# Kernel tuning notes

Hardware: AMD Instinct MI355X
Metric: run time of the kernel (lower is better)

## Reference

```python
import jax, jax.numpy as jnp
import numpy as np

EPS_NORM = 1e-12  # F.normalize eps
EPS_BN = 1e-5     # BatchNorm2d eps


def _neighbor_idx(h, w):
    # Replicates get_window_mask's clamped 3x3 neighbor indices (hw, 9).
    off = np.array([-1, 0, 1])
    x_off = np.tile(off, 3)        # [-1,0,1,-1,0,1,-1,0,1]
    y_off = np.repeat(off, 3)      # [-1,-1,-1,0,0,0,1,1,1]
    yy, xx = np.meshgrid(np.arange(h), np.arange(w), indexing='ij')
    x_nn = np.clip(xx.reshape(-1, 1) + x_off[None, :], 0, w - 1)
    y_nn = np.clip(yy.reshape(-1, 1) + y_off[None, :], 0, h - 1)
    return jnp.asarray(y_nn * w + x_nn, dtype=jnp.int32)  # (hw, 9)


def _find_nn(xf, yf, idx):
    # Faithful to find_nn: cosine sim between cur pixel and 3x3 window of y,
    # argmin over the (masked-in) window, gather the NORMALIZED y feature.
    # The dense (hw,hw) matmul + 9999 mask reduces exactly to these 9 candidates.
    b, c, h, w = xf.shape
    xn = xf.reshape(b, c, h * w).transpose(0, 2, 1)  # (b, hw, c)
    xn = xn / jnp.maximum(jnp.linalg.norm(xn, axis=-1, keepdims=True), EPS_NORM)
    yn = yf.reshape(b, c, h * w)
    yn = yn / jnp.maximum(jnp.linalg.norm(yn, axis=1, keepdims=True), EPS_NORM)
    ynt = yn.transpose(0, 2, 1)          # (b, hw, c)
    y_nb = ynt[:, idx, :]                # (b, hw, 9, c) gathered neighbors
    sims = jnp.einsum('bpc,bpkc->bpk', xn, y_nb)  # (b, hw, 9)
    k = jnp.argmin(sims, axis=-1)
    nnv = jnp.take_along_axis(y_nb, k[:, :, None, None], axis=2)[:, :, 0, :]
    return nnv.transpose(0, 2, 1).reshape(b, c, h, w)


def _forward(x, conv_w, bn_gamma, bn_beta):
    h, w = x.shape[-2:]
    prev_f, next_f, cur_f = x[:, 0], x[:, 1], x[:, 2]
    idx = _neighbor_idx(h, w)
    nn_prev = _find_nn(cur_f, prev_f, idx)
    nn_next = _find_nn(cur_f, next_f, idx)
    feat = jnp.concatenate([nn_prev, nn_next, cur_f], axis=1)  # (b, 3c, h, w)
    out = jnp.einsum('oc,bchw->bohw', conv_w, feat)            # 1x1 conv, no bias
    # BatchNorm2d in training mode: per-channel batch stats (biased var)
    mean = out.mean(axis=(0, 2, 3), keepdims=True)
    var = out.var(axis=(0, 2, 3), keepdims=True)
    out = (out - mean) * jax.lax.rsqrt(var + EPS_BN)
    out = out * bn_gamma[None, :, None, None] + bn_beta[None, :, None, None]
    out = jax.nn.relu(out)
    return jnp.stack([prev_f, next_f, out], axis=1)  # (b, 3, c, h, w)


def setup_inputs() -> dict:
    key = jax.random.key(0)
    k1, k2 = jax.random.split(key)
    b, c, h, w = 8, 256, 64, 64
    x = jax.random.normal(k1, (b, 3, c, h, w), dtype=jnp.float32)
    fan_in, fan_out = 3 * c, c
    bound = float(np.sqrt(6.0 / (fan_in + fan_out)))  # xavier_uniform
    conv_w = jax.random.uniform(k2, (c, 3 * c), dtype=jnp.float32, minval=-bound, maxval=bound)
    bn_gamma = jnp.ones((c,), dtype=jnp.float32)
    bn_beta = jnp.zeros((c,), dtype=jnp.float32)
    return {'x': x, 'conv_w': conv_w, 'bn_gamma': bn_gamma, 'bn_beta': bn_beta}


def reference(x, conv_w, bn_gamma, bn_beta):
    return _forward(x, conv_w, bn_gamma, bn_beta)
```

## Files before the change

kernel.cpp:

```cpp
#include <hip/hip_runtime.h>

constexpr int B  = 8;
constexpr int C  = 256;
constexpr int Hh = 64;
constexpr int Ww = 64;
constexpr int P  = Hh * Ww;
constexpr int CP = C * P;
constexpr int CT = 3 * C;
constexpr int J  = B * P;

constexpr int DOT_D_OFF = 0;
constexpr int SSQ_D_OFF = 294912;
constexpr int IV_F_OFF  = 655360;
constexpr int SEL_F_OFF = 663552;
constexpr int SIV_F_OFF = 671744;
constexpr int WB_F_OFF  = 679936;

typedef __attribute__((ext_vector_type(8))) short short8;
typedef __attribute__((ext_vector_type(4))) float f32x4;

__device__ inline unsigned short bf16_rne(float f) {
    unsigned u = __float_as_uint(f);
    return (unsigned short)((u + 0x7fffu + ((u >> 16) & 1u)) >> 16);
}
__device__ inline unsigned pack2(float a, float b) {
    return (unsigned)bf16_rne(a) | ((unsigned)bf16_rne(b) << 16);
}

__global__ __launch_bounds__(256) void k_wcvt(const float* __restrict__ Wg,
                                              unsigned short* __restrict__ Wb) {
    int i = blockIdx.x * 256 + threadIdx.x;
    Wb[i] = bf16_rne(Wg[i]);
}

__global__ __launch_bounds__(256) void k_dots(const float* __restrict__ x,
                                              float* __restrict__ out) {
    __shared__ float ys[2][2][6][64];
    __shared__ float cs[2][256];
    const int t     = threadIdx.x;
    const int b     = blockIdx.x >> 4;
    const int strip = blockIdx.x & 15;
    const int chunk = blockIdx.y;
    const int y0 = strip * 4;
    const int ry = t >> 6;
    const int xc = t & 63;
    const int xm = max(xc - 1, 0), xp = min(xc + 1, 63);
    const int c0 = chunk * 64;

    size_t gbase; int l0;
    if (t < 64) {
        gbase = (size_t)(b * 3 + 2) * CP + (size_t)c0 * P + strip * 256 + t * 4;
        l0 = t * 4;
    } else {
        int i   = t - 64;
        int sid = i >= 96;
        int r   = (i - sid * 96) >> 4;
        int x4  = i & 15;
        int yl  = min(max(y0 - 1 + r, 0), Hh - 1);
        gbase = (size_t)(b * 3 + sid) * CP + (size_t)c0 * P + yl * 64 + x4 * 4;
        l0 = (sid * 6 + r) * 64 + x4 * 4;
    }
    float* ysf = &ys[0][0][0][0];
    float* dst0 = (t < 64) ? &cs[0][l0] : &ysf[l0];
    float* dst1 = (t < 64) ? &cs[1][l0] : &ysf[768 + l0];

    double d[2][9] = {{0,0,0,0,0,0,0,0,0},{0,0,0,0,0,0,0,0,0}};
    double qs[2] = {0.0, 0.0};

    f32x4 r0 = *(const f32x4*)(x + gbase);
    f32x4 r1 = *(const f32x4*)(x + gbase + (size_t)P);

    #define COMPUTE(BUF)                                                     \
    {                                                                        \
        double cd = (double)cs[BUF][t];                                      \
        _Pragma("unroll")                                                    \
        for (int s = 0; s < 2; ++s) {                                        \
            const float* Y0 = &ys[BUF][s][ry][0];             \
            const float* Y1 = Y0 + 64;                        \
            const float* Y2 = Y1 + 64;                        \
            d[s][0] = fma(cd, (double)Y0[xm], d[s][0]);                      \
            d[s][1] = fma(cd, (double)Y0[xc], d[s][1]);                      \
            d[s][2] = fma(cd, (double)Y0[xp], d[s][2]);                      \
            d[s][3] = fma(cd, (double)Y1[xm], d[s][3]);                      \
            d[s][4] = fma(cd, (double)Y1[xc], d[s][4]);                      \
            d[s][5] = fma(cd, (double)Y1[xp], d[s][5]);                      \
            d[s][6] = fma(cd, (double)Y2[xm], d[s][6]);                      \
            d[s][7] = fma(cd, (double)Y2[xc], d[s][7]);                      \
            d[s][8] = fma(cd, (double)Y2[xp], d[s][8]);                      \
            double ov = (double)Y1[xc];                                      \
            qs[s] = fma(ov, ov, qs[s]);                                      \
        }                                                                    \
    }

    for (int n = 0; n < 64; n += 2) {
        *(f32x4*)dst0 = r0;
        __syncthreads();
        if (n + 2 < 64)
            r0 = *(const f32x4*)(x + gbase + (size_t)(n + 2) * P);
        COMPUTE(0)
        *(f32x4*)dst1 = r1;
        __syncthreads();
        if (n + 3 < 64)
            r1 = *(const f32x4*)(x + gbase + (size_t)(n + 3) * P);
        COMPUTE(1)
    }
    #undef COMPUTE

    const int p = strip * 256 + t;
    double* db = (double*)(out + (size_t)(b * 3) * CP);
    #pragma unroll
    for (int s = 0; s < 2; ++s) {
        #pragma unroll
        for (int k = 0; k < 9; ++k)
            db[DOT_D_OFF + (size_t)((chunk * 2 + s) * 9 + k) * 4096 + p] = d[s][k];
        db[SSQ_D_OFF + (size_t)(chunk * 2 + s) * 4096 + p] = qs[s];
    }
}

__global__ __launch_bounds__(256) void k_iv(float* __restrict__ out) {
    int gid  = blockIdx.x * 256 + threadIdx.x;
    int side = gid >> 15;
    int j    = gid & (J - 1);
    int b = j >> 12, p = j & (P - 1);
    const double* sb = (const double*)(out + (size_t)(b * 3) * CP) + SSQ_D_OFF;
    double ssum = ((sb[(0 * 2 + side) * 4096 + p]
                  + sb[(1 * 2 + side) * 4096 + p])
                  + sb[(2 * 2 + side) * 4096 + p])
                  + sb[(3 * 2 + side) * 4096 + p];
    float* ivb = out + (size_t)(b * 3) * CP + IV_F_OFF;
    ivb[side * 4096 + p] = 1.0f / fmaxf((float)sqrt(ssum), 1e-12f);
}

__global__ __launch_bounds__(256) void k_sel(float* __restrict__ out) {
    int gid  = blockIdx.x * 256 + threadIdx.x;
    int side = gid >> 15;
    int j    = gid & (J - 1);
    int b = j >> 12, p = j & (P - 1);
    int y = p >> 6, xc = p & 63;

    int nidx[9];
    #pragma unroll
    for (int k = 0; k < 9; ++k) {
        int dy = k / 3 - 1, dx = k % 3 - 1;
        int yy = min(max(y + dy, 0), Hh - 1);
        int xx = min(max(xc + dx, 0), Ww - 1);
        nidx[k] = yy * Ww + xx;
    }

    const double* db  = (const double*)(out + (size_t)(b * 3) * CP) + DOT_D_OFF;
    const float*  ivb = out + (size_t)(b * 3) * CP + IV_F_OFF;

    double best = 0.0; int bi = 0;
    #pragma unroll
    for (int k = 0; k < 9; ++k) {
        double sk = ((db[(size_t)((0 * 2 + side) * 9 + k) * 4096 + p]
                    + db[(size_t)((1 * 2 + side) * 9 + k) * 4096 + p])
                    + db[(size_t)((2 * 2 + side) * 9 + k) * 4096 + p])
                    + db[(size_t)((3 * 2 + side) * 9 + k) * 4096 + p];
        double s = sk * (double)ivb[side * 4096 + nidx[k]];
        if (k == 0 || s < best) { best = s; bi = k; }
    }
    int*   selb = (int*)(out + (size_t)(b * 3) * CP + SEL_F_OFF);
    float* sivb = out + (size_t)(b * 3) * CP + SIV_F_OFF;
    selb[side * 4096 + p] = nidx[bi];
    sivb[side * 4096 + p] = ivb[side * 4096 + nidx[bi]];
}

__global__ __launch_bounds__(512) void k_gemm(const float* __restrict__ x,
                                              const unsigned short* __restrict__ Wb,
                                              float* __restrict__ out) {
    __shared__ unsigned short As[4][256][8];
    __shared__ unsigned short Bs[4][128][8];
    __shared__ int   sel_s[2][128];
    __shared__ float siv_s[2][128];

    const int t  = threadIdx.x;
    const int j0 = blockIdx.x * 128;
    const int b  = j0 >> 12, p0 = j0 & (P - 1);

    if (t < 256) {
        int side = t >> 7, jj = t & 127;
        const int*   selb = (const int*)(out + (size_t)(b * 3) * CP + SEL_F_OFF);
        const float* sivb = out + (size_t)(b * 3) * CP + SIV_F_OFF;
        sel_s[side][jj] = selb[side * 4096 + p0 + jj];
        siv_s[side][jj] = sivb[side * 4096 + p0 + jj];
    }
    __syncthreads();

    const float* prevb = x + (size_t)(b * 3 + 0) * CP;
    const float* nextb = x + (size_t)(b * 3 + 1) * CP;
    const float* curb  = x + (size_t)(b * 3 + 2) * CP;

    const int lane = t & 63, w = t >> 6;
    const int q = lane >> 4, l16 = lane & 15;
    const int m0w = (w & 3) * 64;
    const int n0w = (w >> 2) * 64;

    const int jj = t & 127, kq = (t >> 7) & 3;
    const int ma = t & 255, kh = t >> 8;

    f32x4 acc[4][4];
    #pragma unroll
    for (int f = 0; f < 4; ++f)
        #pragma unroll
        for (int g = 0; g < 4; ++g)
            acc[f][g] = (f32x4){0.f, 0.f, 0.f, 0.f};

    for (int kk = 0; kk < CT; kk += 32) {
        const unsigned short* wsrc = Wb + (size_t)ma * CT + kk + kh * 16;
        short8 wa0 = *(const short8*)wsrc;
        short8 wa1 = *(const short8*)(wsrc + 8);

        const float* src; float scale;
        int k0 = kq * 8;
        if (kk < 256) {
            src = prevb + (size_t)(kk + k0) * P + sel_s[0][jj];
            scale = siv_s[0][jj];
        } else if (kk < 512) {
            src = nextb + (size_t)(kk - 256 + k0) * P + sel_s[1][jj];
            scale = siv_s[1][jj];
        } else {
            src = curb + (size_t)(kk - 512 + k0) * P + p0 + jj;
            scale = 1.0f;
        }
        float f0 = src[0] * scale,             f1 = src[(size_t)P] * scale;
        float f2 = src[(size_t)2 * P] * scale, f3 = src[(size_t)3 * P] * scale;
        float f4 = src[(size_t)4 * P] * scale, f5 = src[(size_t)5 * P] * scale;
        float f6 = src[(size_t)6 * P] * scale, f7 = src[(size_t)7 * P] * scale;

        __syncthreads();

        *(short8*)&As[kh * 2    ][ma][0] = wa0;
        *(short8*)&As[kh * 2 + 1][ma][0] = wa1;
        uint4 pk = make_uint4(pack2(f0, f1), pack2(f2, f3),
                              pack2(f4, f5), pack2(f6, f7));
        *(uint4*)&Bs[kq][jj][0] = pk;

        __syncthreads();

        short8 af[4], bfr[4];
        #pragma unroll
        for (int f = 0; f < 4; ++f)
            af[f] = *(const short8*)&As[q][m0w + f * 16 + l16][0];
        #pragma unroll
        for (int g = 0; g < 4; ++g)
            bfr[g] = *(const short8*)&Bs[q][n0w + g * 16 + l16][0];
        #pragma unroll
        for (int f = 0; f < 4; ++f)
            #pragma unroll
            for (int g = 0; g < 4; ++g)
                acc[f][g] = __builtin_amdgcn_mfma_f32_16x16x32_bf16(
                    af[f], bfr[g], acc[f][g], 0, 0, 0);
    }

    float* outb = out + (size_t)(b * 3 + 2) * CP;
    #pragma unroll
    for (int f = 0; f < 4; ++f)
        #pragma unroll
        for (int g = 0; g < 4; ++g)
            #pragma unroll
            for (int r = 0; r < 4; ++r) {
                int ch  = m0w + f * 16 + q * 4 + r;
                int col = p0 + n0w + g * 16 + l16;
                outb[(size_t)ch * P + col] = acc[f][g][r];
            }
}

__global__ __launch_bounds__(256) void k_bn(float* __restrict__ out,
                                            const float* __restrict__ gamma,
                                            const float* __restrict__ beta) {
    __shared__ double rs[256], rq[256];
    __shared__ float sc_s, sh_s;
    const int o = blockIdx.x, t = threadIdx.x;

    double s = 0.0, q = 0.0;
    for (int b = 0; b < B; ++b) {
        const float4* base =
            (const float4*)(out + (size_t)(b * 3 + 2) * CP + (size_t)o * P);
        #pragma unroll
        for (int i = 0; i < 4; ++i) {
            float4 v = base[i * 256 + t];
            s += (double)v.x + (double)v.y + (double)v.z + (double)v.w;
            q += (double)v.x * v.x + (double)v.y * v.y
               + (double)v.z * v.z + (double)v.w * v.w;
        }
    }
    rs[t] = s; rq[t] = q;
    __syncthreads();
    for (int off = 128; off > 0; off >>= 1) {
        if (t < off) { rs[t] += rs[t + off]; rq[t] += rq[t + off]; }
        __syncthreads();
    }
    if (t == 0) {
        double mean = rs[0] * (1.0 / (double)J);
        double var  = rq[0] * (1.0 / (double)J) - mean * mean;
        double inv  = 1.0 / sqrt(var + 1e-5);
        double sc   = (double)gamma[o] * inv;
        sc_s = (float)sc;
        sh_s = (float)((double)beta[o] - mean * sc);
    }
    __syncthreads();
    const float sc = sc_s, sh = sh_s;

    for (int b = 0; b < B; ++b) {
        float4* base =
            (float4*)(out + (size_t)(b * 3 + 2) * CP + (size_t)o * P);
        #pragma unroll
        for (int i = 0; i < 4; ++i) {
            float4 v = base[i * 256 + t];
            v.x = fmaxf(fmaf(v.x, sc, sh), 0.f);
            v.y = fmaxf(fmaf(v.y, sc, sh), 0.f);
            v.z = fmaxf(fmaf(v.z, sc, sh), 0.f);
            v.w = fmaxf(fmaf(v.w, sc, sh), 0.f);
            base[i * 256 + t] = v;
        }
    }
}

__global__ __launch_bounds__(256) void k_copy(const float4* __restrict__ x4,
                                              float4* __restrict__ o4) {
    int tid = blockIdx.x * blockDim.x + threadIdx.x;
    const int per_b = 2 * CP / 4;
    const int bstr  = 3 * CP / 4;
    if (tid < B * per_b) {
        int b = tid / per_b;
        int r = tid - b * per_b;
        o4[b * bstr + r] = x4[b * bstr + r];
    }
}

extern "C" void kernel_launch(void* const* d_in, const int* in_sizes, int n_in,
                              void* d_out, int out_size, void* d_ws, size_t ws_size,
                              hipStream_t stream) {
    const float* x     = (const float*)d_in[0];
    const float* wconv = (const float*)d_in[1];
    const float* gamma = (const float*)d_in[2];
    const float* beta  = (const float*)d_in[3];
    float* out = (float*)d_out;
    (void)d_ws; (void)ws_size;

    unsigned short* Wbuf = (unsigned short*)(out + WB_F_OFF);

    k_wcvt<<<CT * C / 256, 256, 0, stream>>>(wconv, Wbuf);

    k_dots<<<dim3(128, 4), 256, 0, stream>>>(x, out);

    k_iv<<<2 * J / 256, 256, 0, stream>>>(out);

    k_sel<<<2 * J / 256, 256, 0, stream>>>(out);

    k_gemm<<<J / 128, 512, 0, stream>>>(x, Wbuf, out);

    k_bn<<<C, 256, 0, stream>>>(out, gamma, beta);

    k_copy<<<(B * 2 * CP / 4 + 255) / 256, 256, 0, stream>>>(
        (const float4*)x, (float4*)out);
}
```

Measured before the change: 268.7 us.

## Double-buffer GEMM shared-memory tiles to overlap global loads with MFMA

The gather-GEMM kernel now keeps two LDS buffers for the weight and activation tiles. The global loads for the next K step are issued before the MFMAs on the current buffer and written to the other buffer afterward, so only one barrier is needed per iteration. This hides global gather latency behind compute. In exchange it doubles LDS use, which may reduce occupancy, and raises register pressure from holding the prefetched values.

New measurement: 267.5 us. Within noise of the previous version (-0.5%).

```diff
diff --git a/kernel.cpp b/kernel.cpp
--- a/kernel.cpp
+++ b/kernel.cpp
@@ -169,8 +169,8 @@
 __global__ __launch_bounds__(512) void k_gemm(const float* __restrict__ x,
                                               const unsigned short* __restrict__ Wb,
                                               float* __restrict__ out) {
-    __shared__ unsigned short As[4][256][8];
-    __shared__ unsigned short Bs[4][128][8];
+    __shared__ unsigned short As[2][4][256][8];
+    __shared__ unsigned short Bs[2][4][128][8];
     __shared__ int   sel_s[2][128];
     __shared__ float siv_s[2][128];
 
@@ -187,10 +187,6 @@
     }
     __syncthreads();
 
-    const float* prevb = x + (size_t)(b * 3 + 0) * CP;
-    const float* nextb = x + (size_t)(b * 3 + 1) * CP;
-    const float* curb  = x + (size_t)(b * 3 + 2) * CP;
-
     const int lane = t & 63, w = t >> 6;
     const int q = lane >> 4, l16 = lane & 15;
     const int m0w = (w & 3) * 64;
@@ -198,6 +194,13 @@
 
     const int jj = t & 127, kq = (t >> 7) & 3;
     const int ma = t & 255, kh = t >> 8;
+    const int k0 = kq * 8;
+
+    const float* pp = x + (size_t)(b * 3 + 0) * CP + sel_s[0][jj];
+    const float* np = x + (size_t)(b * 3 + 1) * CP + sel_s[1][jj];
+    const float* cp = x + (size_t)(b * 3 + 2) * CP + p0 + jj;
+    const float  sp = siv_s[0][jj], sn = siv_s[1][jj];
+    const unsigned short* wbase = Wb + (size_t)ma * CT + kh * 16;
 
     f32x4 acc[4][4];
     #pragma unroll
@@ -206,52 +209,59 @@
         for (int g = 0; g < 4; ++g)
             acc[f][g] = (f32x4){0.f, 0.f, 0.f, 0.f};
 
-    for (int kk = 0; kk < CT; kk += 32) {
-        const unsigned short* wsrc = Wb + (size_t)ma * CT + kk + kh * 16;
-        short8 wa0 = *(const short8*)wsrc;
-        short8 wa1 = *(const short8*)(wsrc + 8);
-
-        const float* src; float scale;
-        int k0 = kq * 8;
-        if (kk < 256) {
-            src = prevb + (size_t)(kk + k0) * P + sel_s[0][jj];
-            scale = siv_s[0][jj];
-        } else if (kk < 512) {
-            src = nextb + (size_t)(kk - 256 + k0) * P + sel_s[1][jj];
-            scale = siv_s[1][jj];
-        } else {
-            src = curb + (size_t)(kk - 512 + k0) * P + p0 + jj;
-            scale = 1.0f;
-        }
-        float f0 = src[0] * scale,             f1 = src[(size_t)P] * scale;
-        float f2 = src[(size_t)2 * P] * scale, f3 = src[(size_t)3 * P] * scale;
-        float f4 = src[(size_t)4 * P] * scale, f5 = src[(size_t)5 * P] * scale;
-        float f6 = src[(size_t)6 * P] * scale, f7 = src[(size_t)7 * P] * scale;
-
-        __syncthreads();
-
-        *(short8*)&As[kh * 2    ][ma][0] = wa0;
-        *(short8*)&As[kh * 2 + 1][ma][0] = wa1;
-        uint4 pk = make_uint4(pack2(f0, f1), pack2(f2, f3),
-                              pack2(f4, f5), pack2(f6, f7));
-        *(uint4*)&Bs[kq][jj][0] = pk;
-
-        __syncthreads();
-
+    short8 wa0, wa1;
+    float fb[8];
+    float scale;
+
+    #define LOAD_STEP(KK)                                                    \
+    {                                                                        \
+        const unsigned short* wsrc = wbase + (KK);                           \
+        wa0 = *(const short8*)wsrc;                                          \
+        wa1 = *(const short8*)(wsrc + 8);                                    \
+        const float* src;                                                    \
+        if ((KK) < 256)      { src = pp + (size_t)((KK) + k0) * P;       scale = sp;   } \
+        else if ((KK) < 512) { src = np + (size_t)((KK) - 256 + k0) * P; scale = sn;   } \
+        else                 { src = cp + (size_t)((KK) - 512 + k0) * P; scale = 1.0f; } \
+        _Pragma("unroll")                                                    \
+        for (int u = 0; u < 8; ++u) fb[u] = src[(size_t)u * P];              \
+    }
+
+    #define WRITE_STEP(BUF)                                                  \
+    {                                                                        \
+        *(short8*)&As[BUF][kh * 2    ][ma][0] = wa0;                         \
+        *(short8*)&As[BUF][kh * 2 + 1][ma][0] = wa1;                         \
+        uint4 pk = make_uint4(pack2(fb[0] * scale, fb[1] * scale),           \
+                              pack2(fb[2] * scale, fb[3] * scale),           \
+                              pack2(fb[4] * scale, fb[5] * scale),           \
+                              pack2(fb[6] * scale, fb[7] * scale));          \
+        *(uint4*)&Bs[BUF][kq][jj][0] = pk;                                   \
+    }
+
+    LOAD_STEP(0)
+    WRITE_STEP(0)
+    __syncthreads();
+
+    for (int i = 0; i < 24; ++i) {
+        if (i + 1 < 24) LOAD_STEP((i + 1) * 32)
+        const int cur = i & 1;
         short8 af[4], bfr[4];
         #pragma unroll
         for (int f = 0; f < 4; ++f)
-            af[f] = *(const short8*)&As[q][m0w + f * 16 + l16][0];
+            af[f] = *(const short8*)&As[cur][q][m0w + f * 16 + l16][0];
         #pragma unroll
         for (int g = 0; g < 4; ++g)
-            bfr[g] = *(const short8*)&Bs[q][n0w + g * 16 + l16][0];
+            bfr[g] = *(const short8*)&Bs[cur][q][n0w + g * 16 + l16][0];
         #pragma unroll
         for (int f = 0; f < 4; ++f)
             #pragma unroll
             for (int g = 0; g < 4; ++g)
                 acc[f][g] = __builtin_amdgcn_mfma_f32_16x16x32_bf16(
                     af[f], bfr[g], acc[f][g], 0, 0, 0);
-    }
+        if (i + 1 < 24) WRITE_STEP((i + 1) & 1)
+        __syncthreads();
+    }
+    #undef LOAD_STEP
+    #undef WRITE_STEP
 
     float* outb = out + (size_t)(b * 3 + 2) * CP;
     #pragma unroll
```
